# Optimization experiments

Hardware: AMD Instinct MI355X
Metric: run time of the kernel (lower is better)

The kernel has to match this reference:

```python
import jax, jax.numpy as jnp
import numpy as np

# Spiking time schedule: B_n = (1+0.5)*X_n = 1500 per spiking layer (X_n=1000),
# chained via set_params: layer k has t_min = 1500*k, t_max = 1500*(k+1).
B_N = 1500.0


def _region_idx(H, W):
    # 0=center, 1=TL, 2=top, 3=TR, 4=right, 5=BR, 6=bottom, 7=BL, 8=left
    r = np.zeros((H, W), np.int32)
    r[0, :] = 2; r[-1, :] = 6; r[:, 0] = 8; r[:, -1] = 4
    r[0, 0] = 1; r[0, -1] = 3; r[-1, -1] = 5; r[-1, 0] = 7
    return jnp.asarray(r)


def _im2col3(x, t_min):
    # x: [B,H,W,C] -> patches [B,H,W,9*C]; 'same' pad with value t_min
    B, H, W, C = x.shape
    xp = jnp.pad(x, ((0, 0), (1, 1), (1, 1), (0, 0)), constant_values=t_min)
    cols = [xp[:, dy:dy + H, dx:dx + W, :] for dy in range(3) for dx in range(3)]
    return jnp.concatenate(cols, axis=-1)


def _spiking_conv(x, Wk, D, t_min, t_max):
    # ti = (tj - t_min) @ W + (t_max - t_min - D_region) + t_min, clamped at t_max
    p = _im2col3(x, t_min)                       # [B,H,W,9C]
    lin = jnp.einsum('bhwk,kf->bhwf', p - t_min, Wk)
    Dmap = D[_region_idx(x.shape[1], x.shape[2])]  # [H,W,F] border-aware thresholds
    return jnp.minimum(lin + (t_max - Dmap), t_max)


def _spiking_dense(x, Wk, D, t_min, t_max):
    return jnp.minimum((x - t_min) @ Wk + (t_max - D), t_max)


def _pool2(x):
    B, H, W, C = x.shape
    return x.reshape(B, H // 2, 2, W // 2, 2, C).max(axis=(2, 4))


def _forward(x, Wc1, Dc1, Wc2, Dc2, Wc3, Dc3, Wc4, Dc4, Wd1, Dd1, Wout, Dout):
    x = _spiking_conv(x, Wc1, Dc1, 0.0, 1500.0)
    x = _spiking_conv(x, Wc2, Dc2, 1500.0, 3000.0)
    x = _pool2(x)
    x = _spiking_conv(x, Wc3, Dc3, 3000.0, 4500.0)
    x = _spiking_conv(x, Wc4, Dc4, 4500.0, 6000.0)
    x = _pool2(x)
    x = x.reshape(x.shape[0], -1)                 # [B, 16*16*128]
    x = _spiking_dense(x, Wd1, Dd1, 6000.0, 7500.0)
    # output layer: alpha*(t_min - t_min_prev) + (t_min - tj)@W == D_i + (t_min - tj)@W
    return Dout + (7500.0 - x) @ Wout


def setup_inputs() -> dict:
    key = jax.random.key(0)
    ks = jax.random.split(key, 14)
    B, H, C0 = 32, 64, 1

    def w(k, fan_in, fan_out):
        return (jax.random.normal(k, (fan_in, fan_out), jnp.float32)
                / np.float32(np.sqrt(fan_in)))

    def d(k, shape):
        return jax.random.uniform(k, shape, jnp.float32) * 10.0

    return {
        'x': jax.random.uniform(ks[0], (B, H, H, C0), jnp.float32),
        'Wc1': w(ks[1], 9 * C0, 64),    'Dc1': d(ks[2], (9, 64)),
        'Wc2': w(ks[3], 9 * 64, 64),    'Dc2': d(ks[4], (9, 64)),
        'Wc3': w(ks[5], 9 * 64, 128),   'Dc3': d(ks[6], (9, 128)),
        'Wc4': w(ks[7], 9 * 128, 128),  'Dc4': d(ks[8], (9, 128)),
        'Wd1': w(ks[9], 16 * 16 * 128, 256), 'Dd1': d(ks[10], (256,)),
        'Wout': w(ks[11], 256, 10),     'Dout': d(ks[12], (10,)),
    }


def reference(x, Wc1, Dc1, Wc2, Dc2, Wc3, Dc3, Wc4, Dc4, Wd1, Dd1, Wout, Dout):
    return _forward(x, Wc1, Dc1, Wc2, Dc2, Wc3, Dc3, Wc4, Dc4, Wd1, Dd1, Wout, Dout)
```

## Files before the change

### kernel.cpp

```cpp
#include <hip/hip_runtime.h>
#include <hip/hip_bf16.h>

#define DEVINL __device__ __forceinline__

typedef __attribute__((ext_vector_type(8)))  short short8;
typedef __attribute__((ext_vector_type(4)))  float float4v;

DEVINL float bf2f(unsigned short u) { return __uint_as_float(((unsigned)u) << 16); }
DEVINL unsigned short f2bf(float f) {
  unsigned u = __float_as_uint(f);
  unsigned r = u + 0x7FFFu + ((u >> 16) & 1u);
  return (unsigned short)(r >> 16);
}

DEVINL int region_of(int h, int w, int n) {
  if (h == 0)     return (w == 0) ? 1 : ((w == n-1) ? 3 : 2);
  if (h == n-1)   return (w == 0) ? 7 : ((w == n-1) ? 5 : 6);
  return (w == 0) ? 8 : ((w == n-1) ? 4 : 0);
}

__global__ void sentinel_k(float* out, float v) {
  int t = blockIdx.x*64 + threadIdx.x;
  if (t < 320) out[t] = v;
}

__global__ void wtrans_all(const float* __restrict__ W2, const float* __restrict__ W3,
                           const float* __restrict__ W4,
                           unsigned short* __restrict__ T2, unsigned short* __restrict__ T3,
                           unsigned short* __restrict__ T4)
{
  int y = blockIdx.y;
  const float* W = (y == 0) ? W2 : (y == 1) ? W3 : W4;
  unsigned short* T = (y == 0) ? T2 : (y == 1) ? T3 : T4;
  int Ksteps = (y == 2) ? 36 : 18;
  int NT = (y == 0) ? 4 : 8;
  int F  = (y == 0) ? 64 : 128;
  int i = blockIdx.x*256 + threadIdx.x;
  if (i >= Ksteps*NT*64) return;
  int lane = i & 63, nt = (i >> 6) % NT, kstep = i / (64*NT);
  int f = nt*16 + (lane & 15);
  int kbase = kstep*32 + (lane >> 4)*8;
  unsigned short v[8];
  #pragma unroll
  for (int j = 0; j < 8; j++) v[j] = f2bf(W[(kbase + j)*F + f]);
  ushort4* q = (ushort4*)&T[(size_t)i * 8];
  q[0] = make_ushort4(v[0], v[1], v[2], v[3]);
  q[1] = make_ushort4(v[4], v[5], v[6], v[7]);
}

__global__ __launch_bounds__(256) void conv12_k(const float* __restrict__ x,
    const float* __restrict__ Wf1, const float* __restrict__ Df1,
    const unsigned short* __restrict__ Wt, const float* __restrict__ Df2,
    unsigned short* __restrict__ out)
{
  constexpr int Cpad = 72;
  __shared__ __align__(16) unsigned short u[4*66*Cpad];
  __shared__ float xs[6][66];

  int b = blockIdx.y, hp = blockIdx.x, t = threadIdx.x;
  int h0 = hp * 2;

  for (int idx = t; idx < 6*66; idx += 256) {
    int r = idx / 66, wc = idx % 66;
    int hh = h0 - 2 + r, w = wc - 1;
    float v = 0.f;
    if (hh >= 0 && hh < 64 && w >= 0 && w < 64) v = x[(b*64 + hh)*64 + w];
    xs[r][wc] = v;
  }
  __syncthreads();

  {
    int f2 = (t & 31) * 2, g = t >> 5;
    int r = g & 3, wh = g >> 2;
    int hh = h0 - 1 + r;
    bool valid = (hh >= 0 && hh < 64);
    float wka[9], wkb[9];
    #pragma unroll
    for (int k = 0; k < 9; k++) {
      wka[k] = Wf1[k*64 + f2];
      wkb[k] = Wf1[k*64 + f2 + 1];
    }
    int w0 = wh * 32;
    float cA0 = xs[r+0][w0], cA1 = xs[r+1][w0], cA2 = xs[r+2][w0];
    float cB0 = xs[r+0][w0+1], cB1 = xs[r+1][w0+1], cB2 = xs[r+2][w0+1];
    for (int wi = 0; wi < 32; wi++) {
      int w = w0 + wi;
      float cC0 = xs[r+0][w+2], cC1 = xs[r+1][w+2], cC2 = xs[r+2][w+2];
      float aa = cA0*wka[0] + cB0*wka[1] + cC0*wka[2]
               + cA1*wka[3] + cB1*wka[4] + cC1*wka[5]
               + cA2*wka[6] + cB2*wka[7] + cC2*wka[8];
      float ab = cA0*wkb[0] + cB0*wkb[1] + cC0*wkb[2]
               + cA1*wkb[3] + cB1*wkb[4] + cC1*wkb[5]
               + cA2*wkb[6] + cB2*wkb[7] + cC2*wkb[8];
      float va = 0.f, vb = 0.f;
      if (valid) {
        int reg = region_of(hh, w, 64);
        va = fminf(aa - Df1[reg*64 + f2],     0.f);
        vb = fminf(ab - Df1[reg*64 + f2 + 1], 0.f);
      }
      unsigned pk = (unsigned)f2bf(va) | ((unsigned)f2bf(vb) << 16);
      *(unsigned*)&u[(r*66 + (w+1))*Cpad + f2] = pk;
      cA0 = cB0; cB0 = cC0; cA1 = cB1; cB1 = cC1; cA2 = cB2; cB2 = cC2;
    }
    *(unsigned*)&u[(r*66 + (wh ? 65 : 0))*Cpad + f2] = 0u;
  }
  __syncthreads();

  int lane = t & 63, wave = t >> 6;
  int wm = wave >> 1, wn = wave & 1;
  int quad = lane >> 4, lm = lane & 15;

  union ABu { float4 f4; short8 v; };

  float4v acc[2][2][2];
  #pragma unroll
  for (int hi = 0; hi < 2; hi++)
    #pragma unroll
    for (int m = 0; m < 2; m++)
      #pragma unroll
      for (int n = 0; n < 2; n++)
        acc[hi][m][n] = (float4v){0.f, 0.f, 0.f, 0.f};

  #pragma unroll
  for (int dy = 0; dy < 3; dy++)
  #pragma unroll
  for (int dx = 0; dx < 3; dx++)
  #pragma unroll
  for (int c0 = 0; c0 < 64; c0 += 32) {
    int kstep = (dy*3 + dx)*2 + (c0 >> 5);
    ABu bfr[2];
    #pragma unroll
    for (int n = 0; n < 2; n++)
      bfr[n].f4 = *(const float4*)&Wt[(size_t)((kstep*4 + wn*2 + n)*64 + lane)*8];
    #pragma unroll
    for (int hi = 0; hi < 2; hi++) {
      ABu afr[2];
      #pragma unroll
      for (int m = 0; m < 2; m++)
        afr[m].f4 = *(const float4*)&u[((hi+dy)*66 + ((wm*2 + m)*16 + lm + dx))*Cpad + c0 + quad*8];
      #pragma unroll
      for (int n = 0; n < 2; n++)
        #pragma unroll
        for (int m = 0; m < 2; m++)
          acc[hi][m][n] = __builtin_amdgcn_mfma_f32_16x16x32_bf16(afr[m].v, bfr[n].v, acc[hi][m][n], 0, 0, 0);
    }
  }

  #pragma unroll
  for (int m = 0; m < 2; m++)
    #pragma unroll
    for (int n = 0; n < 2; n++) {
      int mm = wm*2 + m;
      int f = (wn*2 + n)*16 + lm;
      #pragma unroll
      for (int rp = 0; rp < 2; rp++) {
        float mx = -1e30f;
        #pragma unroll
        for (int hi = 0; hi < 2; hi++)
          #pragma unroll
          for (int rr = 0; rr < 2; rr++) {
            int h = h0 + hi, w = mm*16 + quad*4 + 2*rp + rr;
            float v = fminf(acc[hi][m][n][2*rp+rr] - Df2[region_of(h, w, 64)*64 + f], 0.f);
            mx = fmaxf(mx, v);
          }
        int wp = mm*8 + quad*2 + rp;
        out[(((size_t)b*32 + hp)*32 + wp)*64 + f] = f2bf(mx);
      }
    }
}

template<int C, int F, int N, bool POOL, int WSM>
__global__ __launch_bounds__(256) void conv_mfma(
    const unsigned short* __restrict__ U, const unsigned short* __restrict__ Wt,
    const float* __restrict__ Df, unsigned short* __restrict__ out)
{
  constexpr int RC   = POOL ? 2 : 1;
  constexpr int ROWS = RC + 2;
  constexpr int Cpad = C + 8;
  constexpr int NT = F / 16;
  constexpr int MT = N / 16;
  constexpr int WSN = 4 / WSM;
  constexpr int MW = MT / WSM;
  constexpr int NW = NT / WSN;

  __shared__ __align__(16) unsigned short lds[ROWS*(N+2)*Cpad];

  int b = blockIdx.y, hp = blockIdx.x, t = threadIdx.x;
  int h0 = hp * RC;

  const int stage16 = ROWS*(N+2)*(C/8);
  #pragma unroll 4
  for (int i = t; i < stage16; i += 256) {
    int c8 = i % (C/8), wc = (i/(C/8)) % (N+2), r = i/((C/8)*(N+2));
    int hh = h0 - 1 + r, w = wc - 1;
    float4 v = make_float4(0.f,0.f,0.f,0.f);
    if (hh >= 0 && hh < N && w >= 0 && w < N)
      v = *(const float4*)&U[(((size_t)b*N + hh)*N + w)*C + c8*8];
    *(float4*)&lds[(r*(N+2) + wc)*Cpad + c8*8] = v;
  }
  __syncthreads();

  int lane = t & 63, wave = t >> 6;
  int wm = wave / WSN, wn = wave % WSN;
  int quad = lane >> 4, lm = lane & 15;

  union ABu { float4 f4; short8 v; };

  float4v acc[RC][MW][NW];
  #pragma unroll
  for (int hi = 0; hi < RC; hi++)
    #pragma unroll
    for (int m = 0; m < MW; m++)
      #pragma unroll
      for (int n = 0; n < NW; n++)
        acc[hi][m][n] = (float4v){0.f, 0.f, 0.f, 0.f};

  #pragma unroll
  for (int dy = 0; dy < 3; dy++)
  #pragma unroll
  for (int dx = 0; dx < 3; dx++)
  #pragma unroll
  for (int c0 = 0; c0 < C; c0 += 32) {
    int kstep = (dy*3 + dx)*(C/32) + (c0 >> 5);
    ABu bfr[NW];
    #pragma unroll
    for (int n = 0; n < NW; n++)
      bfr[n].f4 = *(const float4*)&Wt[(size_t)((kstep*NT + wn*NW + n)*64 + lane)*8];
    #pragma unroll
    for (int hi = 0; hi < RC; hi++) {
      ABu afr[MW];
      #pragma unroll
      for (int m = 0; m < MW; m++)
        afr[m].f4 = *(const float4*)&lds[((hi+dy)*(N+2) + ((wm*MW + m)*16 + lm + dx))*Cpad + c0 + quad*8];
      #pragma unroll
      for (int n = 0; n < NW; n++)
        #pragma unroll
        for (int m = 0; m < MW; m++)
          acc[hi][m][n] = __builtin_amdgcn_mfma_f32_16x16x32_bf16(afr[m].v, bfr[n].v, acc[hi][m][n], 0, 0, 0);
    }
  }

  if constexpr (POOL) {
    constexpr int M2 = N/2;
    #pragma unroll
    for (int m = 0; m < MW; m++)
      #pragma unroll
      for (int n = 0; n < NW; n++) {
        int mm = wm*MW + m;
        int f = (wn*NW + n)*16 + lm;
        #pragma unroll
        for (int rp = 0; rp < 2; rp++) {
          float mx = -1e30f;
          #pragma unroll
          for (int hi = 0; hi < 2; hi++)
            #pragma unroll
            for (int rr = 0; rr < 2; rr++) {
              int h = h0 + hi, w = mm*16 + quad*4 + 2*rp + rr;
              float v = fminf(acc[hi][m][n][2*rp+rr] - Df[region_of(h, w, N)*F + f], 0.f);
              mx = fmaxf(mx, v);
            }
          int wp = mm*8 + quad*2 + rp;
          out[(((size_t)b*M2 + hp)*M2 + wp)*F + f] = f2bf(mx);
        }
      }
  } else {
    int h = h0;
    #pragma unroll
    for (int m = 0; m < MW; m++)
      #pragma unroll
      for (int n = 0; n < NW; n++) {
        int mm = wm*MW + m;
        int f = (wn*NW + n)*16 + lm;
        #pragma unroll
        for (int r = 0; r < 4; r++) {
          int w = mm*16 + quad*4 + r;
          int reg = region_of(h, w, N);
          float v = fminf(acc[0][m][n][r] - Df[reg*F + f], 0.f);
          out[(((size_t)b*N + h)*N + w)*F + f] = f2bf(v);
        }
      }
  }
}

__global__ __launch_bounds__(256) void dense_k(const unsigned short* __restrict__ act,
    const float* __restrict__ W, float* __restrict__ part)
{
  int blk = blockIdx.x, t = threadIdx.x;
  int kblk = blk >> 1, fh = blk & 1;
  int k0 = kblk * 128;
  __shared__ float a[128][36];
  for (int idx = t; idx < 32*128; idx += 256) {
    int bb = idx >> 7, kc = idx & 127;
    a[kc][bb] = bf2f(act[(size_t)bb*32768 + k0 + kc]);
  }
  __syncthreads();
  int f0 = fh*128 + (t & 31)*4, b0 = (t >> 5)*4;
  float acc[4][4] = {};
  #pragma unroll 8
  for (int kc = 0; kc < 128; kc++) {
    float4 wv = *(const float4*)&W[(size_t)(k0 + kc)*256 + f0];
    float4 av = *(const float4*)&a[kc][b0];
    const float* avp = (const float*)&av;
    #pragma unroll
    for (int bb = 0; bb < 4; bb++) {
      float avx = avp[bb];
      acc[bb][0] += avx * wv.x;
      acc[bb][1] += avx * wv.y;
      acc[bb][2] += avx * wv.z;
      acc[bb][3] += avx * wv.w;
    }
  }
  #pragma unroll
  for (int bb = 0; bb < 4; bb++) {
    float4 v = make_float4(acc[bb][0], acc[bb][1], acc[bb][2], acc[bb][3]);
    *(float4*)&part[(size_t)kblk*8192 + (b0+bb)*256 + f0] = v;
  }
}

__global__ __launch_bounds__(1024) void redfin_k(const float* __restrict__ part,
    const float* __restrict__ Dd, const float* __restrict__ Wo,
    const float* __restrict__ Do, float* __restrict__ out)
{
  int b = blockIdx.x, t = threadIdx.x;
  int f = t & 255, kq = t >> 8;
  float s = 0.f;
  #pragma unroll 16
  for (int blk = kq*64; blk < kq*64 + 64; blk++)
    s += part[(size_t)blk*8192 + b*256 + f];
  __shared__ float red[4][256];
  red[kq][f] = s;
  __syncthreads();
  __shared__ float ud[256];
  if (t < 256) {
    float v = red[0][t] + red[1][t] + red[2][t] + red[3][t];
    ud[t] = fminf(v - Dd[t], 0.f);
  }
  __syncthreads();
  int lane = t & 63, wave = t >> 6;
  if (wave < 4) {
    for (int o = wave; o < 10; o += 4) {
      float acc = 0.f;
      #pragma unroll
      for (int j = 0; j < 4; j++) {
        int ff = j*64 + lane;
        acc += ud[ff] * Wo[ff*10 + o];
      }
      #pragma unroll
      for (int off = 32; off; off >>= 1) acc += __shfl_down(acc, off, 64);
      if (lane == 0) out[b*10 + o] = Do[o] - acc;
    }
  }
}

extern "C" void kernel_launch(void* const* d_in, const int* in_sizes, int n_in,
                              void* d_out, int out_size, void* d_ws, size_t ws_size,
                              hipStream_t stream)
{
  float* outp = (float*)d_out;

  if (n_in != 13) { sentinel_k<<<5, 64, 0, stream>>>(outp, 200.f); return; }
  const int exp_sz[13] = {131072, 576, 576, 36864, 576, 73728, 1152,
                          147456, 1152, 8388608, 256, 2560, 10};
  for (int i = 0; i < 13; i++)
    if (in_sizes[i] != exp_sz[i]) {
      sentinel_k<<<5, 64, 0, stream>>>(outp, 1000.f + 100.f*i); return;
    }
  if (ws_size < (37u << 20)) { sentinel_k<<<5, 64, 0, stream>>>(outp, 500.f); return; }

  char* wsb = (char*)d_ws;
  const float* x    = (const float*)d_in[0];
  const float* Wc1  = (const float*)d_in[1];
  const float* Dc1  = (const float*)d_in[2];
  const float* Wc2  = (const float*)d_in[3];
  const float* Dc2  = (const float*)d_in[4];
  const float* Wc3  = (const float*)d_in[5];
  const float* Dc3  = (const float*)d_in[6];
  const float* Wc4  = (const float*)d_in[7];
  const float* Dc4  = (const float*)d_in[8];
  const float* Wd1  = (const float*)d_in[9];
  const float* Dd1  = (const float*)d_in[10];
  const float* Wout = (const float*)d_in[11];
  const float* Dout = (const float*)d_in[12];

  unsigned short* Wt2 = (unsigned short*)(wsb + (1u << 20));
  unsigned short* Wt3 = (unsigned short*)(wsb + (1u << 20) + 262144);
  unsigned short* Wt4 = (unsigned short*)(wsb + (1u << 20) + 524288);
  unsigned short* P2 = (unsigned short*)(wsb + (19u << 20));
  unsigned short* U3 = (unsigned short*)(wsb + (2u  << 20));
  unsigned short* P4 = (unsigned short*)(wsb + (19u << 20));
  float* part        = (float*)(wsb + (2u  << 20));

  wtrans_all<<<dim3(72, 3), 256, 0, stream>>>(Wc2, Wc3, Wc4, Wt2, Wt3, Wt4);
  conv12_k<<<dim3(32, 32), 256, 0, stream>>>(x, Wc1, Dc1, Wt2, Dc2, P2);
  conv_mfma<64, 128, 32, false, 1><<<dim3(32, 32), 256, 0, stream>>>(P2, Wt3, Dc3, U3);
  conv_mfma<128, 128, 32, true, 1><<<dim3(16, 32), 256, 0, stream>>>(U3, Wt4, Dc4, P4);
  dense_k<<<512, 256, 0, stream>>>(P4, Wd1, part);
  redfin_k<<<32, 1024, 0, stream>>>(part, Dd1, Wout, Dout, outp);
}
```

Measured before the change: 163.0 us.

## Fuse conv3 and conv4+pool into one kernel keeping conv3 rows in LDS

Replaces the two separate conv_mfma launches with a single conv34_k. Each block computes four conv3 rows, including a one-row halo on each side, into LDS in bf16, then runs conv4 with 2x2 max-pooling directly from that LDS tile. This removes the U3 global write and read round-trip and one kernel launch. The cost is recomputing the halo rows (double the conv3 work) with only 512 blocks and a larger LDS footprint, which may reduce occupancy. The dense loop unroll is also raised from 8 to 16.

```diff
diff --git a/kernel.cpp b/kernel.cpp
--- a/kernel.cpp
+++ b/kernel.cpp
@@ -169,85 +169,130 @@
     }
 }
 
-template<int C, int F, int N, bool POOL, int WSM>
-__global__ __launch_bounds__(256) void conv_mfma(
-    const unsigned short* __restrict__ U, const unsigned short* __restrict__ Wt,
-    const float* __restrict__ Df, unsigned short* __restrict__ out)
-{
-  constexpr int RC   = POOL ? 2 : 1;
-  constexpr int ROWS = RC + 2;
-  constexpr int Cpad = C + 8;
-  constexpr int NT = F / 16;
-  constexpr int MT = N / 16;
-  constexpr int WSN = 4 / WSM;
-  constexpr int MW = MT / WSM;
-  constexpr int NW = NT / WSN;
-
-  __shared__ __align__(16) unsigned short lds[ROWS*(N+2)*Cpad];
-
-  int b = blockIdx.y, hp = blockIdx.x, t = threadIdx.x;
-  int h0 = hp * RC;
-
-  const int stage16 = ROWS*(N+2)*(C/8);
+__global__ __launch_bounds__(256) void conv34_k(
+    const unsigned short* __restrict__ P2, const unsigned short* __restrict__ Wt3,
+    const float* __restrict__ Df3, const unsigned short* __restrict__ Wt4,
+    const float* __restrict__ Df4, unsigned short* __restrict__ out)
+{
+  __shared__ __align__(16) unsigned short p2[6*34*72];
+  __shared__ __align__(16) unsigned short u3[4*34*136];
+
+  int b = blockIdx.y, hp4 = blockIdx.x, t = threadIdx.x;
+  int h30 = hp4*2 - 1;
+
   #pragma unroll 4
-  for (int i = t; i < stage16; i += 256) {
-    int c8 = i % (C/8), wc = (i/(C/8)) % (N+2), r = i/((C/8)*(N+2));
-    int hh = h0 - 1 + r, w = wc - 1;
+  for (int i = t; i < 6*34*8; i += 256) {
+    int c8 = i & 7, wc = (i >> 3) % 34, r = i / (8*34);
+    int hh = h30 - 1 + r, w = wc - 1;
     float4 v = make_float4(0.f,0.f,0.f,0.f);
-    if (hh >= 0 && hh < N && w >= 0 && w < N)
-      v = *(const float4*)&U[(((size_t)b*N + hh)*N + w)*C + c8*8];
-    *(float4*)&lds[(r*(N+2) + wc)*Cpad + c8*8] = v;
-  }
+    if (hh >= 0 && hh < 32 && w >= 0 && w < 32)
+      v = *(const float4*)&P2[(((size_t)b*32 + hh)*32 + w)*64 + c8*8];
+    *(float4*)&p2[(r*34 + wc)*72 + c8*8] = v;
+  }
+  for (int i = t; i < 4*34*136/2; i += 256) ((unsigned*)u3)[i] = 0u;
   __syncthreads();
 
   int lane = t & 63, wave = t >> 6;
-  int wm = wave / WSN, wn = wave % WSN;
   int quad = lane >> 4, lm = lane & 15;
-
   union ABu { float4 f4; short8 v; };
 
-  float4v acc[RC][MW][NW];
-  #pragma unroll
-  for (int hi = 0; hi < RC; hi++)
-    #pragma unroll
-    for (int m = 0; m < MW; m++)
-      #pragma unroll
-      for (int n = 0; n < NW; n++)
-        acc[hi][m][n] = (float4v){0.f, 0.f, 0.f, 0.f};
-
-  #pragma unroll
-  for (int dy = 0; dy < 3; dy++)
-  #pragma unroll
-  for (int dx = 0; dx < 3; dx++)
-  #pragma unroll
-  for (int c0 = 0; c0 < C; c0 += 32) {
-    int kstep = (dy*3 + dx)*(C/32) + (c0 >> 5);
-    ABu bfr[NW];
-    #pragma unroll
-    for (int n = 0; n < NW; n++)
-      bfr[n].f4 = *(const float4*)&Wt[(size_t)((kstep*NT + wn*NW + n)*64 + lane)*8];
-    #pragma unroll
-    for (int hi = 0; hi < RC; hi++) {
-      ABu afr[MW];
-      #pragma unroll
-      for (int m = 0; m < MW; m++)
-        afr[m].f4 = *(const float4*)&lds[((hi+dy)*(N+2) + ((wm*MW + m)*16 + lm + dx))*Cpad + c0 + quad*8];
-      #pragma unroll
-      for (int n = 0; n < NW; n++)
-        #pragma unroll
-        for (int m = 0; m < MW; m++)
-          acc[hi][m][n] = __builtin_amdgcn_mfma_f32_16x16x32_bf16(afr[m].v, bfr[n].v, acc[hi][m][n], 0, 0, 0);
-    }
-  }
-
-  if constexpr (POOL) {
-    constexpr int M2 = N/2;
-    #pragma unroll
-    for (int m = 0; m < MW; m++)
-      #pragma unroll
-      for (int n = 0; n < NW; n++) {
-        int mm = wm*MW + m;
-        int f = (wn*NW + n)*16 + lm;
+  {
+    float4v acc[4][2][2];
+    #pragma unroll
+    for (int r = 0; r < 4; r++)
+      #pragma unroll
+      for (int m = 0; m < 2; m++)
+        #pragma unroll
+        for (int n = 0; n < 2; n++)
+          acc[r][m][n] = (float4v){0.f,0.f,0.f,0.f};
+
+    #pragma unroll
+    for (int dy = 0; dy < 3; dy++)
+    #pragma unroll
+    for (int dx = 0; dx < 3; dx++)
+    #pragma unroll
+    for (int c0 = 0; c0 < 64; c0 += 32) {
+      int kstep = (dy*3+dx)*2 + (c0 >> 5);
+      ABu bfr[2];
+      #pragma unroll
+      for (int n = 0; n < 2; n++)
+        bfr[n].f4 = *(const float4*)&Wt3[(size_t)((kstep*8 + wave*2 + n)*64 + lane)*8];
+      #pragma unroll
+      for (int r = 0; r < 4; r++) {
+        ABu afr[2];
+        #pragma unroll
+        for (int m = 0; m < 2; m++)
+          afr[m].f4 = *(const float4*)&p2[((r+dy)*34 + (m*16 + lm + dx))*72 + c0 + quad*8];
+        #pragma unroll
+        for (int n = 0; n < 2; n++)
+          #pragma unroll
+          for (int m = 0; m < 2; m++)
+            acc[r][m][n] = __builtin_amdgcn_mfma_f32_16x16x32_bf16(afr[m].v, bfr[n].v, acc[r][m][n], 0,0,0);
+      }
+    }
+    #pragma unroll
+    for (int r = 0; r < 4; r++) {
+      int h3 = h30 + r;
+      if (h3 >= 0 && h3 < 32) {
+        #pragma unroll
+        for (int m = 0; m < 2; m++)
+          #pragma unroll
+          for (int n = 0; n < 2; n++) {
+            int f = (wave*2 + n)*16 + lm;
+            #pragma unroll
+            for (int rr = 0; rr < 4; rr++) {
+              int w = m*16 + quad*4 + rr;
+              float v = fminf(acc[r][m][n][rr] - Df3[region_of(h3, w, 32)*128 + f], 0.f);
+              u3[(r*34 + (w+1))*136 + f] = f2bf(v);
+            }
+          }
+      }
+    }
+  }
+  __syncthreads();
+
+  {
+    int wn = wave;
+    int h0 = hp4*2;
+    float4v acc[2][2][2];
+    #pragma unroll
+    for (int hi = 0; hi < 2; hi++)
+      #pragma unroll
+      for (int m = 0; m < 2; m++)
+        #pragma unroll
+        for (int n = 0; n < 2; n++)
+          acc[hi][m][n] = (float4v){0.f,0.f,0.f,0.f};
+
+    #pragma unroll
+    for (int dy = 0; dy < 3; dy++)
+    #pragma unroll
+    for (int dx = 0; dx < 3; dx++)
+    #pragma unroll
+    for (int c0 = 0; c0 < 128; c0 += 32) {
+      int kstep = (dy*3+dx)*4 + (c0 >> 5);
+      ABu bfr[2];
+      #pragma unroll
+      for (int n = 0; n < 2; n++)
+        bfr[n].f4 = *(const float4*)&Wt4[(size_t)((kstep*8 + wn*2 + n)*64 + lane)*8];
+      #pragma unroll
+      for (int hi = 0; hi < 2; hi++) {
+        ABu afr[2];
+        #pragma unroll
+        for (int m = 0; m < 2; m++)
+          afr[m].f4 = *(const float4*)&u3[((hi+dy)*34 + (m*16 + lm + dx))*136 + c0 + quad*8];
+        #pragma unroll
+        for (int n = 0; n < 2; n++)
+          #pragma unroll
+          for (int m = 0; m < 2; m++)
+            acc[hi][m][n] = __builtin_amdgcn_mfma_f32_16x16x32_bf16(afr[m].v, bfr[n].v, acc[hi][m][n], 0,0,0);
+      }
+    }
+
+    #pragma unroll
+    for (int m = 0; m < 2; m++)
+      #pragma unroll
+      for (int n = 0; n < 2; n++) {
+        int f = (wn*2 + n)*16 + lm;
         #pragma unroll
         for (int rp = 0; rp < 2; rp++) {
           float mx = -1e30f;
@@ -255,28 +300,12 @@
           for (int hi = 0; hi < 2; hi++)
             #pragma unroll
             for (int rr = 0; rr < 2; rr++) {
-              int h = h0 + hi, w = mm*16 + quad*4 + 2*rp + rr;
-              float v = fminf(acc[hi][m][n][2*rp+rr] - Df[region_of(h, w, N)*F + f], 0.f);
+              int h = h0 + hi, w = m*16 + quad*4 + 2*rp + rr;
+              float v = fminf(acc[hi][m][n][2*rp+rr] - Df4[region_of(h, w, 32)*128 + f], 0.f);
               mx = fmaxf(mx, v);
             }
-          int wp = mm*8 + quad*2 + rp;
-          out[(((size_t)b*M2 + hp)*M2 + wp)*F + f] = f2bf(mx);
-        }
-      }
-  } else {
-    int h = h0;
-    #pragma unroll
-    for (int m = 0; m < MW; m++)
-      #pragma unroll
-      for (int n = 0; n < NW; n++) {
-        int mm = wm*MW + m;
-        int f = (wn*NW + n)*16 + lm;
-        #pragma unroll
-        for (int r = 0; r < 4; r++) {
-          int w = mm*16 + quad*4 + r;
-          int reg = region_of(h, w, N);
-          float v = fminf(acc[0][m][n][r] - Df[reg*F + f], 0.f);
-          out[(((size_t)b*N + h)*N + w)*F + f] = f2bf(v);
+          int wp = m*8 + quad*2 + rp;
+          out[(((size_t)b*16 + hp4)*16 + wp)*128 + f] = f2bf(mx);
         }
       }
   }
@@ -296,7 +325,7 @@
   __syncthreads();
   int f0 = fh*128 + (t & 31)*4, b0 = (t >> 5)*4;
   float acc[4][4] = {};
-  #pragma unroll 8
+  #pragma unroll 16
   for (int kc = 0; kc < 128; kc++) {
     float4 wv = *(const float4*)&W[(size_t)(k0 + kc)*256 + f0];
     float4 av = *(const float4*)&a[kc][b0];
@@ -385,15 +414,13 @@
   unsigned short* Wt2 = (unsigned short*)(wsb + (1u << 20));
   unsigned short* Wt3 = (unsigned short*)(wsb + (1u << 20) + 262144);
   unsigned short* Wt4 = (unsigned short*)(wsb + (1u << 20) + 524288);
-  unsigned short* P2 = (unsigned short*)(wsb + (19u << 20));
-  unsigned short* U3 = (unsigned short*)(wsb + (2u  << 20));
-  unsigned short* P4 = (unsigned short*)(wsb + (19u << 20));
-  float* part        = (float*)(wsb + (2u  << 20));
+  unsigned short* P2  = (unsigned short*)(wsb + (19u << 20));
+  unsigned short* P4  = (unsigned short*)(wsb + (25u << 20));
+  float* part         = (float*)(wsb + (2u  << 20));
 
   wtrans_all<<<dim3(72, 3), 256, 0, stream>>>(Wc2, Wc3, Wc4, Wt2, Wt3, Wt4);
   conv12_k<<<dim3(32, 32), 256, 0, stream>>>(x, Wc1, Dc1, Wt2, Dc2, P2);
-  conv_mfma<64, 128, 32, false, 1><<<dim3(32, 32), 256, 0, stream>>>(P2, Wt3, Dc3, U3);
-  conv_mfma<128, 128, 32, true, 1><<<dim3(16, 32), 256, 0, stream>>>(U3, Wt4, Dc4, P4);
+  conv34_k<<<dim3(16, 32), 256, 0, stream>>>(P2, Wt3, Dc3, Wt4, Dc4, P4);
   dense_k<<<512, 256, 0, stream>>>(P4, Wd1, part);
   redfin_k<<<32, 1024, 0, stream>>>(part, Dd1, Wout, Dout, outp);
 }
```

Result: slower. 174.2 us (+6.9%).

## Retile conv waves: one M tile by four N tiles, two output rows per block

Applied to the files above, without the earlier changes.

The fused conv1/conv2 kernel now gives each wave one 16-pixel M tile and all four 16-filter N tiles, replacing the 2x2 wave split, so each A fragment is reused across four MFMAs. The generic conv_mfma is replaced by conv_hf, where each block computes two output rows and each wave covers 16 pixels by 64 filters. conv3 therefore runs half as many blocks and stages the input halo once for two rows instead of one. The dense kernel's unroll goes from 8 to 16, and P4 moves to its own workspace offset. More accumulators per wave and fewer blocks may lower occupancy and latency hiding.

```diff
diff --git a/kernel.cpp b/kernel.cpp
--- a/kernel.cpp
+++ b/kernel.cpp
@@ -107,19 +107,16 @@
   __syncthreads();
 
   int lane = t & 63, wave = t >> 6;
-  int wm = wave >> 1, wn = wave & 1;
   int quad = lane >> 4, lm = lane & 15;
 
   union ABu { float4 f4; short8 v; };
 
-  float4v acc[2][2][2];
+  float4v acc[2][4];
   #pragma unroll
   for (int hi = 0; hi < 2; hi++)
     #pragma unroll
-    for (int m = 0; m < 2; m++)
-      #pragma unroll
-      for (int n = 0; n < 2; n++)
-        acc[hi][m][n] = (float4v){0.f, 0.f, 0.f, 0.f};
+    for (int n = 0; n < 4; n++)
+      acc[hi][n] = (float4v){0.f, 0.f, 0.f, 0.f};
 
   #pragma unroll
   for (int dy = 0; dy < 3; dy++)
@@ -128,30 +125,103 @@
   #pragma unroll
   for (int c0 = 0; c0 < 64; c0 += 32) {
     int kstep = (dy*3 + dx)*2 + (c0 >> 5);
-    ABu bfr[2];
-    #pragma unroll
-    for (int n = 0; n < 2; n++)
-      bfr[n].f4 = *(const float4*)&Wt[(size_t)((kstep*4 + wn*2 + n)*64 + lane)*8];
-    #pragma unroll
-    for (int hi = 0; hi < 2; hi++) {
-      ABu afr[2];
-      #pragma unroll
-      for (int m = 0; m < 2; m++)
-        afr[m].f4 = *(const float4*)&u[((hi+dy)*66 + ((wm*2 + m)*16 + lm + dx))*Cpad + c0 + quad*8];
-      #pragma unroll
-      for (int n = 0; n < 2; n++)
+    ABu bfr[4];
+    #pragma unroll
+    for (int n = 0; n < 4; n++)
+      bfr[n].f4 = *(const float4*)&Wt[(size_t)((kstep*4 + n)*64 + lane)*8];
+    ABu afr[2];
+    #pragma unroll
+    for (int hi = 0; hi < 2; hi++)
+      afr[hi].f4 = *(const float4*)&u[((hi+dy)*66 + (wave*16 + lm + dx))*Cpad + c0 + quad*8];
+    #pragma unroll
+    for (int hi = 0; hi < 2; hi++)
+      #pragma unroll
+      for (int n = 0; n < 4; n++)
+        acc[hi][n] = __builtin_amdgcn_mfma_f32_16x16x32_bf16(afr[hi].v, bfr[n].v, acc[hi][n], 0, 0, 0);
+  }
+
+  #pragma unroll
+  for (int n = 0; n < 4; n++) {
+    int f = n*16 + lm;
+    #pragma unroll
+    for (int rp = 0; rp < 2; rp++) {
+      float mx = -1e30f;
+      #pragma unroll
+      for (int hi = 0; hi < 2; hi++)
         #pragma unroll
-        for (int m = 0; m < 2; m++)
-          acc[hi][m][n] = __builtin_amdgcn_mfma_f32_16x16x32_bf16(afr[m].v, bfr[n].v, acc[hi][m][n], 0, 0, 0);
-    }
-  }
-
-  #pragma unroll
-  for (int m = 0; m < 2; m++)
-    #pragma unroll
-    for (int n = 0; n < 2; n++) {
-      int mm = wm*2 + m;
-      int f = (wn*2 + n)*16 + lm;
+        for (int rr = 0; rr < 2; rr++) {
+          int h = h0 + hi, w = wave*16 + quad*4 + 2*rp + rr;
+          float v = fminf(acc[hi][n][2*rp+rr] - Df2[region_of(h, w, 64)*64 + f], 0.f);
+          mx = fmaxf(mx, v);
+        }
+      int wp = wave*8 + quad*2 + rp;
+      out[(((size_t)b*32 + hp)*32 + wp)*64 + f] = f2bf(mx);
+    }
+  }
+}
+
+template<int C, bool POOL>
+__global__ __launch_bounds__(256) void conv_hf(
+    const unsigned short* __restrict__ U, const unsigned short* __restrict__ Wt,
+    const float* __restrict__ Df, unsigned short* __restrict__ out)
+{
+  constexpr int Cpad = C + 8;
+
+  __shared__ __align__(16) unsigned short lds[4*34*Cpad];
+
+  int b = blockIdx.y, hp = blockIdx.x, t = threadIdx.x;
+  int h0 = hp * 2;
+
+  const int stage16 = 4*34*(C/8);
+  #pragma unroll 4
+  for (int i = t; i < stage16; i += 256) {
+    int c8 = i % (C/8), wc = (i/(C/8)) % 34, r = i/((C/8)*34);
+    int hh = h0 - 1 + r, w = wc - 1;
+    float4 v = make_float4(0.f,0.f,0.f,0.f);
+    if (hh >= 0 && hh < 32 && w >= 0 && w < 32)
+      v = *(const float4*)&U[(((size_t)b*32 + hh)*32 + w)*C + c8*8];
+    *(float4*)&lds[(r*34 + wc)*Cpad + c8*8] = v;
+  }
+  __syncthreads();
+
+  int lane = t & 63, wave = t >> 6;
+  int m = wave >> 1, fh = wave & 1;
+  int quad = lane >> 4, lm = lane & 15;
+  union ABu { float4 f4; short8 v; };
+
+  float4v acc[2][4];
+  #pragma unroll
+  for (int hi = 0; hi < 2; hi++)
+    #pragma unroll
+    for (int n = 0; n < 4; n++)
+      acc[hi][n] = (float4v){0.f, 0.f, 0.f, 0.f};
+
+  #pragma unroll
+  for (int dy = 0; dy < 3; dy++)
+  #pragma unroll
+  for (int dx = 0; dx < 3; dx++)
+  #pragma unroll
+  for (int c0 = 0; c0 < C; c0 += 32) {
+    int kstep = (dy*3 + dx)*(C/32) + (c0 >> 5);
+    ABu bfr[4];
+    #pragma unroll
+    for (int n = 0; n < 4; n++)
+      bfr[n].f4 = *(const float4*)&Wt[(size_t)((kstep*8 + fh*4 + n)*64 + lane)*8];
+    ABu afr[2];
+    #pragma unroll
+    for (int hi = 0; hi < 2; hi++)
+      afr[hi].f4 = *(const float4*)&lds[((hi+dy)*34 + (m*16 + lm + dx))*Cpad + c0 + quad*8];
+    #pragma unroll
+    for (int hi = 0; hi < 2; hi++)
+      #pragma unroll
+      for (int n = 0; n < 4; n++)
+        acc[hi][n] = __builtin_amdgcn_mfma_f32_16x16x32_bf16(afr[hi].v, bfr[n].v, acc[hi][n], 0, 0, 0);
+  }
+
+  if constexpr (POOL) {
+    #pragma unroll
+    for (int n = 0; n < 4; n++) {
+      int f = fh*64 + n*16 + lm;
       #pragma unroll
       for (int rp = 0; rp < 2; rp++) {
         float mx = -1e30f;
@@ -159,126 +229,29 @@
         for (int hi = 0; hi < 2; hi++)
           #pragma unroll
           for (int rr = 0; rr < 2; rr++) {
-            int h = h0 + hi, w = mm*16 + quad*4 + 2*rp + rr;
-            float v = fminf(acc[hi][m][n][2*rp+rr] - Df2[region_of(h, w, 64)*64 + f], 0.f);
+            int h = h0 + hi, w = m*16 + quad*4 + 2*rp + rr;
+            float v = fminf(acc[hi][n][2*rp+rr] - Df[region_of(h, w, 32)*128 + f], 0.f);
             mx = fmaxf(mx, v);
           }
-        int wp = mm*8 + quad*2 + rp;
-        out[(((size_t)b*32 + hp)*32 + wp)*64 + f] = f2bf(mx);
+        int wp = m*8 + quad*2 + rp;
+        out[(((size_t)b*16 + hp)*16 + wp)*128 + f] = f2bf(mx);
       }
     }
-}
-
-template<int C, int F, int N, bool POOL, int WSM>
-__global__ __launch_bounds__(256) void conv_mfma(
-    const unsigned short* __restrict__ U, const unsigned short* __restrict__ Wt,
-    const float* __restrict__ Df, unsigned short* __restrict__ out)
-{
-  constexpr int RC   = POOL ? 2 : 1;
-  constexpr int ROWS = RC + 2;
-  constexpr int Cpad = C + 8;
-  constexpr int NT = F / 16;
-  constexpr int MT = N / 16;
-  constexpr int WSN = 4 / WSM;
-  constexpr int MW = MT / WSM;
-  constexpr int NW = NT / WSN;
-
-  __shared__ __align__(16) unsigned short lds[ROWS*(N+2)*Cpad];
-
-  int b = blockIdx.y, hp = blockIdx.x, t = threadIdx.x;
-  int h0 = hp * RC;
-
-  const int stage16 = ROWS*(N+2)*(C/8);
-  #pragma unroll 4
-  for (int i = t; i < stage16; i += 256) {
-    int c8 = i % (C/8), wc = (i/(C/8)) % (N+2), r = i/((C/8)*(N+2));
-    int hh = h0 - 1 + r, w = wc - 1;
-    float4 v = make_float4(0.f,0.f,0.f,0.f);
-    if (hh >= 0 && hh < N && w >= 0 && w < N)
-      v = *(const float4*)&U[(((size_t)b*N + hh)*N + w)*C + c8*8];
-    *(float4*)&lds[(r*(N+2) + wc)*Cpad + c8*8] = v;
-  }
-  __syncthreads();
-
-  int lane = t & 63, wave = t >> 6;
-  int wm = wave / WSN, wn = wave % WSN;
-  int quad = lane >> 4, lm = lane & 15;
-
-  union ABu { float4 f4; short8 v; };
-
-  float4v acc[RC][MW][NW];
-  #pragma unroll
-  for (int hi = 0; hi < RC; hi++)
-    #pragma unroll
-    for (int m = 0; m < MW; m++)
-      #pragma unroll
-      for (int n = 0; n < NW; n++)
-        acc[hi][m][n] = (float4v){0.f, 0.f, 0.f, 0.f};
-
-  #pragma unroll
-  for (int dy = 0; dy < 3; dy++)
-  #pragma unroll
-  for (int dx = 0; dx < 3; dx++)
-  #pragma unroll
-  for (int c0 = 0; c0 < C; c0 += 32) {
-    int kstep = (dy*3 + dx)*(C/32) + (c0 >> 5);
-    ABu bfr[NW];
-    #pragma unroll
-    for (int n = 0; n < NW; n++)
-      bfr[n].f4 = *(const float4*)&Wt[(size_t)((kstep*NT + wn*NW + n)*64 + lane)*8];
-    #pragma unroll
-    for (int hi = 0; hi < RC; hi++) {
-      ABu afr[MW];
-      #pragma unroll
-      for (int m = 0; m < MW; m++)
-        afr[m].f4 = *(const float4*)&lds[((hi+dy)*(N+2) + ((wm*MW + m)*16 + lm + dx))*Cpad + c0 + quad*8];
-      #pragma unroll
-      for (int n = 0; n < NW; n++)
+  } else {
+    #pragma unroll
+    for (int hi = 0; hi < 2; hi++) {
+      int h = h0 + hi;
+      #pragma unroll
+      for (int n = 0; n < 4; n++) {
+        int f = fh*64 + n*16 + lm;
         #pragma unroll
-        for (int m = 0; m < MW; m++)
-          acc[hi][m][n] = __builtin_amdgcn_mfma_f32_16x16x32_bf16(afr[m].v, bfr[n].v, acc[hi][m][n], 0, 0, 0);
-    }
-  }
-
-  if constexpr (POOL) {
-    constexpr int M2 = N/2;
-    #pragma unroll
-    for (int m = 0; m < MW; m++)
-      #pragma unroll
-      for (int n = 0; n < NW; n++) {
-        int mm = wm*MW + m;
-        int f = (wn*NW + n)*16 + lm;
-        #pragma unroll
-        for (int rp = 0; rp < 2; rp++) {
-          float mx = -1e30f;
-          #pragma unroll
-          for (int hi = 0; hi < 2; hi++)
-            #pragma unroll
-            for (int rr = 0; rr < 2; rr++) {
-              int h = h0 + hi, w = mm*16 + quad*4 + 2*rp + rr;
-              float v = fminf(acc[hi][m][n][2*rp+rr] - Df[region_of(h, w, N)*F + f], 0.f);
-              mx = fmaxf(mx, v);
-            }
-          int wp = mm*8 + quad*2 + rp;
-          out[(((size_t)b*M2 + hp)*M2 + wp)*F + f] = f2bf(mx);
+        for (int r = 0; r < 4; r++) {
+          int w = m*16 + quad*4 + r;
+          float v = fminf(acc[hi][n][r] - Df[region_of(h, w, 32)*128 + f], 0.f);
+          out[(((size_t)b*32 + h)*32 + w)*128 + f] = f2bf(v);
         }
       }
-  } else {
-    int h = h0;
-    #pragma unroll
-    for (int m = 0; m < MW; m++)
-      #pragma unroll
-      for (int n = 0; n < NW; n++) {
-        int mm = wm*MW + m;
-        int f = (wn*NW + n)*16 + lm;
-        #pragma unroll
-        for (int r = 0; r < 4; r++) {
-          int w = mm*16 + quad*4 + r;
-          int reg = region_of(h, w, N);
-          float v = fminf(acc[0][m][n][r] - Df[reg*F + f], 0.f);
-          out[(((size_t)b*N + h)*N + w)*F + f] = f2bf(v);
-        }
-      }
+    }
   }
 }
 
@@ -296,7 +269,7 @@
   __syncthreads();
   int f0 = fh*128 + (t & 31)*4, b0 = (t >> 5)*4;
   float acc[4][4] = {};
-  #pragma unroll 8
+  #pragma unroll 16
   for (int kc = 0; kc < 128; kc++) {
     float4 wv = *(const float4*)&W[(size_t)(k0 + kc)*256 + f0];
     float4 av = *(const float4*)&a[kc][b0];
@@ -385,15 +358,15 @@
   unsigned short* Wt2 = (unsigned short*)(wsb + (1u << 20));
   unsigned short* Wt3 = (unsigned short*)(wsb + (1u << 20) + 262144);
   unsigned short* Wt4 = (unsigned short*)(wsb + (1u << 20) + 524288);
-  unsigned short* P2 = (unsigned short*)(wsb + (19u << 20));
-  unsigned short* U3 = (unsigned short*)(wsb + (2u  << 20));
-  unsigned short* P4 = (unsigned short*)(wsb + (19u << 20));
-  float* part        = (float*)(wsb + (2u  << 20));
+  unsigned short* P2  = (unsigned short*)(wsb + (19u << 20));
+  unsigned short* U3  = (unsigned short*)(wsb + (2u  << 20));
+  unsigned short* P4  = (unsigned short*)(wsb + (25u << 20));
+  float* part         = (float*)(wsb + (2u  << 20));
 
   wtrans_all<<<dim3(72, 3), 256, 0, stream>>>(Wc2, Wc3, Wc4, Wt2, Wt3, Wt4);
   conv12_k<<<dim3(32, 32), 256, 0, stream>>>(x, Wc1, Dc1, Wt2, Dc2, P2);
-  conv_mfma<64, 128, 32, false, 1><<<dim3(32, 32), 256, 0, stream>>>(P2, Wt3, Dc3, U3);
-  conv_mfma<128, 128, 32, true, 1><<<dim3(16, 32), 256, 0, stream>>>(U3, Wt4, Dc4, P4);
+  conv_hf<64,  false><<<dim3(16, 32), 256, 0, stream>>>(P2, Wt3, Dc3, U3);
+  conv_hf<128, true ><<<dim3(16, 32), 256, 0, stream>>>(U3, Wt4, Dc4, P4);
   dense_k<<<512, 256, 0, stream>>>(P4, Wd1, part);
   redfin_k<<<32, 1024, 0, stream>>>(part, Dd1, Wout, Dout, outp);
 }
```

Result: slower. 169.9 us (+4.2%).

## Process more output rows per block in conv kernels to reuse weight fragments

Applied to the files above, without the earlier changes.

Each conv kernel now computes more output rows per workgroup: conv12 does four rows instead of two, conv3 two rows instead of one, and conv4 four rows instead of two. Each weight fragment loaded from global memory is therefore reused across more MFMA row tiles, and the halo overhead in LDS is smaller. The cost is fewer blocks, more accumulator registers, and larger LDS, which can reduce occupancy. The generic conv template is replaced by a specialized 32-wide one, the dense inner loop is unrolled further, and P4 moves to a separate workspace offset.

```diff
diff --git a/kernel.cpp b/kernel.cpp
--- a/kernel.cpp
+++ b/kernel.cpp
@@ -54,13 +54,13 @@
     unsigned short* __restrict__ out)
 {
   constexpr int Cpad = 72;
-  __shared__ __align__(16) unsigned short u[4*66*Cpad];
-  __shared__ float xs[6][66];
-
-  int b = blockIdx.y, hp = blockIdx.x, t = threadIdx.x;
-  int h0 = hp * 2;
-
-  for (int idx = t; idx < 6*66; idx += 256) {
+  __shared__ __align__(16) unsigned short u[6*66*Cpad];
+  __shared__ float xs[8][66];
+
+  int b = blockIdx.y, hp2 = blockIdx.x, t = threadIdx.x;
+  int h0 = hp2 * 4;
+
+  for (int idx = t; idx < 8*66; idx += 256) {
     int r = idx / 66, wc = idx % 66;
     int hh = h0 - 2 + r, w = wc - 1;
     float v = 0.f;
@@ -71,38 +71,40 @@
 
   {
     int f2 = (t & 31) * 2, g = t >> 5;
-    int r = g & 3, wh = g >> 2;
-    int hh = h0 - 1 + r;
-    bool valid = (hh >= 0 && hh < 64);
     float wka[9], wkb[9];
     #pragma unroll
     for (int k = 0; k < 9; k++) {
       wka[k] = Wf1[k*64 + f2];
       wkb[k] = Wf1[k*64 + f2 + 1];
     }
-    int w0 = wh * 32;
-    float cA0 = xs[r+0][w0], cA1 = xs[r+1][w0], cA2 = xs[r+2][w0];
-    float cB0 = xs[r+0][w0+1], cB1 = xs[r+1][w0+1], cB2 = xs[r+2][w0+1];
-    for (int wi = 0; wi < 32; wi++) {
-      int w = w0 + wi;
-      float cC0 = xs[r+0][w+2], cC1 = xs[r+1][w+2], cC2 = xs[r+2][w+2];
-      float aa = cA0*wka[0] + cB0*wka[1] + cC0*wka[2]
-               + cA1*wka[3] + cB1*wka[4] + cC1*wka[5]
-               + cA2*wka[6] + cB2*wka[7] + cC2*wka[8];
-      float ab = cA0*wkb[0] + cB0*wkb[1] + cC0*wkb[2]
-               + cA1*wkb[3] + cB1*wkb[4] + cC1*wkb[5]
-               + cA2*wkb[6] + cB2*wkb[7] + cC2*wkb[8];
-      float va = 0.f, vb = 0.f;
-      if (valid) {
-        int reg = region_of(hh, w, 64);
-        va = fminf(aa - Df1[reg*64 + f2],     0.f);
-        vb = fminf(ab - Df1[reg*64 + f2 + 1], 0.f);
+    for (int jj = g; jj < 12; jj += 8) {
+      int r = jj >> 1, wh = jj & 1;
+      int hh = h0 - 1 + r;
+      bool valid = (hh >= 0 && hh < 64);
+      int w0 = wh * 32;
+      float cA0 = xs[r+0][w0], cA1 = xs[r+1][w0], cA2 = xs[r+2][w0];
+      float cB0 = xs[r+0][w0+1], cB1 = xs[r+1][w0+1], cB2 = xs[r+2][w0+1];
+      for (int wi = 0; wi < 32; wi++) {
+        int w = w0 + wi;
+        float cC0 = xs[r+0][w+2], cC1 = xs[r+1][w+2], cC2 = xs[r+2][w+2];
+        float aa = cA0*wka[0] + cB0*wka[1] + cC0*wka[2]
+                 + cA1*wka[3] + cB1*wka[4] + cC1*wka[5]
+                 + cA2*wka[6] + cB2*wka[7] + cC2*wka[8];
+        float ab = cA0*wkb[0] + cB0*wkb[1] + cC0*wkb[2]
+                 + cA1*wkb[3] + cB1*wkb[4] + cC1*wkb[5]
+                 + cA2*wkb[6] + cB2*wkb[7] + cC2*wkb[8];
+        float va = 0.f, vb = 0.f;
+        if (valid) {
+          int reg = region_of(hh, w, 64);
+          va = fminf(aa - Df1[reg*64 + f2],     0.f);
+          vb = fminf(ab - Df1[reg*64 + f2 + 1], 0.f);
+        }
+        unsigned pk = (unsigned)f2bf(va) | ((unsigned)f2bf(vb) << 16);
+        *(unsigned*)&u[(r*66 + (w+1))*Cpad + f2] = pk;
+        cA0 = cB0; cB0 = cC0; cA1 = cB1; cB1 = cC1; cA2 = cB2; cB2 = cC2;
       }
-      unsigned pk = (unsigned)f2bf(va) | ((unsigned)f2bf(vb) << 16);
-      *(unsigned*)&u[(r*66 + (w+1))*Cpad + f2] = pk;
-      cA0 = cB0; cB0 = cC0; cA1 = cB1; cB1 = cC1; cA2 = cB2; cB2 = cC2;
-    }
-    *(unsigned*)&u[(r*66 + (wh ? 65 : 0))*Cpad + f2] = 0u;
+      *(unsigned*)&u[(r*66 + (wh ? 65 : 0))*Cpad + f2] = 0u;
+    }
   }
   __syncthreads();
 
@@ -112,9 +114,9 @@
 
   union ABu { float4 f4; short8 v; };
 
-  float4v acc[2][2][2];
-  #pragma unroll
-  for (int hi = 0; hi < 2; hi++)
+  float4v acc[4][2][2];
+  #pragma unroll
+  for (int hi = 0; hi < 4; hi++)
     #pragma unroll
     for (int m = 0; m < 2; m++)
       #pragma unroll
@@ -133,7 +135,7 @@
     for (int n = 0; n < 2; n++)
       bfr[n].f4 = *(const float4*)&Wt[(size_t)((kstep*4 + wn*2 + n)*64 + lane)*8];
     #pragma unroll
-    for (int hi = 0; hi < 2; hi++) {
+    for (int hi = 0; hi < 4; hi++) {
       ABu afr[2];
       #pragma unroll
       for (int m = 0; m < 2; m++)
@@ -153,101 +155,7 @@
       int mm = wm*2 + m;
       int f = (wn*2 + n)*16 + lm;
       #pragma unroll
-      for (int rp = 0; rp < 2; rp++) {
-        float mx = -1e30f;
-        #pragma unroll
-        for (int hi = 0; hi < 2; hi++)
-          #pragma unroll
-          for (int rr = 0; rr < 2; rr++) {
-            int h = h0 + hi, w = mm*16 + quad*4 + 2*rp + rr;
-            float v = fminf(acc[hi][m][n][2*rp+rr] - Df2[region_of(h, w, 64)*64 + f], 0.f);
-            mx = fmaxf(mx, v);
-          }
-        int wp = mm*8 + quad*2 + rp;
-        out[(((size_t)b*32 + hp)*32 + wp)*64 + f] = f2bf(mx);
-      }
-    }
-}
-
-template<int C, int F, int N, bool POOL, int WSM>
-__global__ __launch_bounds__(256) void conv_mfma(
-    const unsigned short* __restrict__ U, const unsigned short* __restrict__ Wt,
-    const float* __restrict__ Df, unsigned short* __restrict__ out)
-{
-  constexpr int RC   = POOL ? 2 : 1;
-  constexpr int ROWS = RC + 2;
-  constexpr int Cpad = C + 8;
-  constexpr int NT = F / 16;
-  constexpr int MT = N / 16;
-  constexpr int WSN = 4 / WSM;
-  constexpr int MW = MT / WSM;
-  constexpr int NW = NT / WSN;
-
-  __shared__ __align__(16) unsigned short lds[ROWS*(N+2)*Cpad];
-
-  int b = blockIdx.y, hp = blockIdx.x, t = threadIdx.x;
-  int h0 = hp * RC;
-
-  const int stage16 = ROWS*(N+2)*(C/8);
-  #pragma unroll 4
-  for (int i = t; i < stage16; i += 256) {
-    int c8 = i % (C/8), wc = (i/(C/8)) % (N+2), r = i/((C/8)*(N+2));
-    int hh = h0 - 1 + r, w = wc - 1;
-    float4 v = make_float4(0.f,0.f,0.f,0.f);
-    if (hh >= 0 && hh < N && w >= 0 && w < N)
-      v = *(const float4*)&U[(((size_t)b*N + hh)*N + w)*C + c8*8];
-    *(float4*)&lds[(r*(N+2) + wc)*Cpad + c8*8] = v;
-  }
-  __syncthreads();
-
-  int lane = t & 63, wave = t >> 6;
-  int wm = wave / WSN, wn = wave % WSN;
-  int quad = lane >> 4, lm = lane & 15;
-
-  union ABu { float4 f4; short8 v; };
-
-  float4v acc[RC][MW][NW];
-  #pragma unroll
-  for (int hi = 0; hi < RC; hi++)
-    #pragma unroll
-    for (int m = 0; m < MW; m++)
-      #pragma unroll
-      for (int n = 0; n < NW; n++)
-        acc[hi][m][n] = (float4v){0.f, 0.f, 0.f, 0.f};
-
-  #pragma unroll
-  for (int dy = 0; dy < 3; dy++)
-  #pragma unroll
-  for (int dx = 0; dx < 3; dx++)
-  #pragma unroll
-  for (int c0 = 0; c0 < C; c0 += 32) {
-    int kstep = (dy*3 + dx)*(C/32) + (c0 >> 5);
-    ABu bfr[NW];
-    #pragma unroll
-    for (int n = 0; n < NW; n++)
-      bfr[n].f4 = *(const float4*)&Wt[(size_t)((kstep*NT + wn*NW + n)*64 + lane)*8];
-    #pragma unroll
-    for (int hi = 0; hi < RC; hi++) {
-      ABu afr[MW];
-      #pragma unroll
-      for (int m = 0; m < MW; m++)
-        afr[m].f4 = *(const float4*)&lds[((hi+dy)*(N+2) + ((wm*MW + m)*16 + lm + dx))*Cpad + c0 + quad*8];
-      #pragma unroll
-      for (int n = 0; n < NW; n++)
-        #pragma unroll
-        for (int m = 0; m < MW; m++)
-          acc[hi][m][n] = __builtin_amdgcn_mfma_f32_16x16x32_bf16(afr[m].v, bfr[n].v, acc[hi][m][n], 0, 0, 0);
-    }
-  }
-
-  if constexpr (POOL) {
-    constexpr int M2 = N/2;
-    #pragma unroll
-    for (int m = 0; m < MW; m++)
-      #pragma unroll
-      for (int n = 0; n < NW; n++) {
-        int mm = wm*MW + m;
-        int f = (wn*NW + n)*16 + lm;
+      for (int hp_loc = 0; hp_loc < 2; hp_loc++)
         #pragma unroll
         for (int rp = 0; rp < 2; rp++) {
           float mx = -1e30f;
@@ -255,30 +163,120 @@
           for (int hi = 0; hi < 2; hi++)
             #pragma unroll
             for (int rr = 0; rr < 2; rr++) {
-              int h = h0 + hi, w = mm*16 + quad*4 + 2*rp + rr;
-              float v = fminf(acc[hi][m][n][2*rp+rr] - Df[region_of(h, w, N)*F + f], 0.f);
+              int h = h0 + 2*hp_loc + hi, w = mm*16 + quad*4 + 2*rp + rr;
+              float v = fminf(acc[2*hp_loc+hi][m][n][2*rp+rr] - Df2[region_of(h, w, 64)*64 + f], 0.f);
               mx = fmaxf(mx, v);
             }
           int wp = mm*8 + quad*2 + rp;
-          out[(((size_t)b*M2 + hp)*M2 + wp)*F + f] = f2bf(mx);
+          out[(((size_t)b*32 + (hp2*2 + hp_loc))*32 + wp)*64 + f] = f2bf(mx);
         }
+    }
+}
+
+template<int C, int RC, bool POOL>
+__global__ __launch_bounds__(256) void conv_rc(
+    const unsigned short* __restrict__ U, const unsigned short* __restrict__ Wt,
+    const float* __restrict__ Df, unsigned short* __restrict__ out)
+{
+  constexpr int Cpad = C + 8;
+  constexpr int ROWS = RC + 2;
+
+  __shared__ __align__(16) unsigned short lds[ROWS*34*Cpad];
+
+  int b = blockIdx.y, hp = blockIdx.x, t = threadIdx.x;
+  int h0 = hp * RC;
+
+  const int stage16 = ROWS*34*(C/8);
+  #pragma unroll 4
+  for (int i = t; i < stage16; i += 256) {
+    int c8 = i % (C/8), wc = (i/(C/8)) % 34, r = i/((C/8)*34);
+    int hh = h0 - 1 + r, w = wc - 1;
+    float4 v = make_float4(0.f,0.f,0.f,0.f);
+    if (hh >= 0 && hh < 32 && w >= 0 && w < 32)
+      v = *(const float4*)&U[(((size_t)b*32 + hh)*32 + w)*C + c8*8];
+    *(float4*)&lds[(r*34 + wc)*Cpad + c8*8] = v;
+  }
+  __syncthreads();
+
+  int lane = t & 63, wave = t >> 6;
+  int wn = wave;
+  int quad = lane >> 4, lm = lane & 15;
+  union ABu { float4 f4; short8 v; };
+
+  float4v acc[RC][2][2];
+  #pragma unroll
+  for (int hi = 0; hi < RC; hi++)
+    #pragma unroll
+    for (int m = 0; m < 2; m++)
+      #pragma unroll
+      for (int n = 0; n < 2; n++)
+        acc[hi][m][n] = (float4v){0.f, 0.f, 0.f, 0.f};
+
+  #pragma unroll
+  for (int dy = 0; dy < 3; dy++)
+  #pragma unroll
+  for (int dx = 0; dx < 3; dx++)
+  #pragma unroll
+  for (int c0 = 0; c0 < C; c0 += 32) {
+    int kstep = (dy*3 + dx)*(C/32) + (c0 >> 5);
+    ABu bfr[2];
+    #pragma unroll
+    for (int n = 0; n < 2; n++)
+      bfr[n].f4 = *(const float4*)&Wt[(size_t)((kstep*8 + wn*2 + n)*64 + lane)*8];
+    #pragma unroll
+    for (int hi = 0; hi < RC; hi++) {
+      ABu afr[2];
+      #pragma unroll
+      for (int m = 0; m < 2; m++)
+        afr[m].f4 = *(const float4*)&lds[((hi+dy)*34 + (m*16 + lm + dx))*Cpad + c0 + quad*8];
+      #pragma unroll
+      for (int n = 0; n < 2; n++)
+        #pragma unroll
+        for (int m = 0; m < 2; m++)
+          acc[hi][m][n] = __builtin_amdgcn_mfma_f32_16x16x32_bf16(afr[m].v, bfr[n].v, acc[hi][m][n], 0, 0, 0);
+    }
+  }
+
+  if constexpr (POOL) {
+    #pragma unroll
+    for (int m = 0; m < 2; m++)
+      #pragma unroll
+      for (int n = 0; n < 2; n++) {
+        int f = (wn*2 + n)*16 + lm;
+        #pragma unroll
+        for (int hp_loc = 0; hp_loc < RC/2; hp_loc++)
+          #pragma unroll
+          for (int rp = 0; rp < 2; rp++) {
+            float mx = -1e30f;
+            #pragma unroll
+            for (int hi = 0; hi < 2; hi++)
+              #pragma unroll
+              for (int rr = 0; rr < 2; rr++) {
+                int h = h0 + 2*hp_loc + hi, w = m*16 + quad*4 + 2*rp + rr;
+                float v = fminf(acc[2*hp_loc+hi][m][n][2*rp+rr] - Df[region_of(h, w, 32)*128 + f], 0.f);
+                mx = fmaxf(mx, v);
+              }
+            int wp = m*8 + quad*2 + rp;
+            out[(((size_t)b*16 + (hp*(RC/2) + hp_loc))*16 + wp)*128 + f] = f2bf(mx);
+          }
       }
   } else {
-    int h = h0;
-    #pragma unroll
-    for (int m = 0; m < MW; m++)
-      #pragma unroll
-      for (int n = 0; n < NW; n++) {
-        int mm = wm*MW + m;
-        int f = (wn*NW + n)*16 + lm;
-        #pragma unroll
-        for (int r = 0; r < 4; r++) {
-          int w = mm*16 + quad*4 + r;
-          int reg = region_of(h, w, N);
-          float v = fminf(acc[0][m][n][r] - Df[reg*F + f], 0.f);
-          out[(((size_t)b*N + h)*N + w)*F + f] = f2bf(v);
+    #pragma unroll
+    for (int hi = 0; hi < RC; hi++) {
+      int h = h0 + hi;
+      #pragma unroll
+      for (int m = 0; m < 2; m++)
+        #pragma unroll
+        for (int n = 0; n < 2; n++) {
+          int f = (wn*2 + n)*16 + lm;
+          #pragma unroll
+          for (int r = 0; r < 4; r++) {
+            int w = m*16 + quad*4 + r;
+            float v = fminf(acc[hi][m][n][r] - Df[region_of(h, w, 32)*128 + f], 0.f);
+            out[(((size_t)b*32 + h)*32 + w)*128 + f] = f2bf(v);
+          }
         }
-      }
+    }
   }
 }
 
@@ -296,7 +294,7 @@
   __syncthreads();
   int f0 = fh*128 + (t & 31)*4, b0 = (t >> 5)*4;
   float acc[4][4] = {};
-  #pragma unroll 8
+  #pragma unroll 16
   for (int kc = 0; kc < 128; kc++) {
     float4 wv = *(const float4*)&W[(size_t)(k0 + kc)*256 + f0];
     float4 av = *(const float4*)&a[kc][b0];
@@ -385,15 +383,15 @@
   unsigned short* Wt2 = (unsigned short*)(wsb + (1u << 20));
   unsigned short* Wt3 = (unsigned short*)(wsb + (1u << 20) + 262144);
   unsigned short* Wt4 = (unsigned short*)(wsb + (1u << 20) + 524288);
-  unsigned short* P2 = (unsigned short*)(wsb + (19u << 20));
-  unsigned short* U3 = (unsigned short*)(wsb + (2u  << 20));
-  unsigned short* P4 = (unsigned short*)(wsb + (19u << 20));
-  float* part        = (float*)(wsb + (2u  << 20));
+  unsigned short* P2  = (unsigned short*)(wsb + (19u << 20));
+  unsigned short* U3  = (unsigned short*)(wsb + (2u  << 20));
+  unsigned short* P4  = (unsigned short*)(wsb + (25u << 20));
+  float* part         = (float*)(wsb + (2u  << 20));
 
   wtrans_all<<<dim3(72, 3), 256, 0, stream>>>(Wc2, Wc3, Wc4, Wt2, Wt3, Wt4);
-  conv12_k<<<dim3(32, 32), 256, 0, stream>>>(x, Wc1, Dc1, Wt2, Dc2, P2);
-  conv_mfma<64, 128, 32, false, 1><<<dim3(32, 32), 256, 0, stream>>>(P2, Wt3, Dc3, U3);
-  conv_mfma<128, 128, 32, true, 1><<<dim3(16, 32), 256, 0, stream>>>(U3, Wt4, Dc4, P4);
+  conv12_k<<<dim3(16, 32), 256, 0, stream>>>(x, Wc1, Dc1, Wt2, Dc2, P2);
+  conv_rc<64,  2, false><<<dim3(16, 32), 256, 0, stream>>>(P2, Wt3, Dc3, U3);
+  conv_rc<128, 4, true ><<<dim3(8, 32), 256, 0, stream>>>(U3, Wt4, Dc4, P4);
   dense_k<<<512, 256, 0, stream>>>(P4, Wd1, part);
   redfin_k<<<32, 1024, 0, stream>>>(part, Dd1, Wout, Dout, outp);
 }
```

Result: slower. 185.2 us (+13.6%).
